# Kernel tuning notes

Measured on AMD Instinct MI355X. Metric: run time of the kernel, lower is better.

Reference implementation:

```python
import jax, jax.numpy as jnp
import numpy as np
from jax import lax

SCALES = [2 ** i for i in range(9)]  # h_grid_global(9, 2**8): dyadic scales 1..256
EPS = 2e-5


def conv1d(x, w, dil, pad):
    # x: [B, Cin, X], w: [Cout, Cin, k]; 'same'-style padding pad on each side, rhs dilation dil
    return lax.conv_general_dilated(x, w, window_strides=(1,), padding=[(pad, pad)],
                                    rhs_dilation=(dil,), dimension_numbers=('NCH', 'OIH', 'NCH'))


def maxpool2_x(x):
    # max pool kernel=2 stride=2 over last (spatial) axis, floor mode like torch
    L = x.shape[-1]
    L2 = (L // 2) * 2
    x = x[..., :L2]
    return jnp.max(x.reshape(x.shape[:-1] + (L2 // 2, 2)), axis=-1)


def lift_conv(x, w):
    k = w.shape[-1]
    outs = [conv1d(x, w, s, s * (k // 2)) / s for s in SCALES]
    return jnp.stack(outs, axis=2)


def gg_conv(x, w):
    # GConvGG with h_crop: x [B, Cin, H, X], w [Cout, Cin, nh=3, k] -> [B, Cout, H-2, X]
    # output scale index i uses input scale slabs i..i+2, x-dilation = scale_i, 1/scale_i normalization
    B, Cin, H, X = x.shape
    Cout, _, nh, k = w.shape
    wf = w.reshape(Cout, Cin * nh, k)
    outs = []
    for i in range(H - nh + 1):
        xi = x[:, :, i:i + nh, :].reshape(B, Cin * nh, X)
        s = SCALES[i]
        outs.append(conv1d(xi, wf, s, s * (k // 2)) / s)
    return jnp.stack(outs, axis=2)


def batchnorm(x, g, b):
    # BatchNorm2d (training batch stats, biased var) over [B, C, H, X]
    m = jnp.mean(x, axis=(0, 2, 3), keepdims=True)
    v = jnp.mean((x - m) ** 2, axis=(0, 2, 3), keepdims=True)
    gb = g[None, :, None, None]
    bb = b[None, :, None, None]
    return gb * (x - m) * lax.rsqrt(v + EPS) + bb


def _winit(key, shape):
    fan = int(np.prod(shape[1:]))
    return jax.random.normal(key, shape, dtype=jnp.float32) * (fan ** -0.5)


def setup_inputs() -> dict:
    key = jax.random.key(0)
    ks = jax.random.split(key, 12)
    B = 4096
    nc = 12
    x = jax.random.normal(ks[0], (B, 100, 6), dtype=jnp.float32)
    inp = {
        'x': x,
        'w1': _winit(ks[1], (nc, 6, 7)),
        'w2': _winit(ks[2], (nc * 2, nc, 3, 5)),
        'w3': _winit(ks[3], (nc * 4, nc * 2, 3, 5)),
        'w4': _winit(ks[4], (nc * 8, nc * 4, 3, 3)),
        'g1': jnp.ones((nc,), jnp.float32), 'b1': jnp.zeros((nc,), jnp.float32),
        'g2': jnp.ones((nc * 2,), jnp.float32), 'b2': jnp.zeros((nc * 2,), jnp.float32),
        'g3': jnp.ones((nc * 4,), jnp.float32), 'b3': jnp.zeros((nc * 4,), jnp.float32),
        'g4': jnp.ones((nc * 8,), jnp.float32), 'b4': jnp.zeros((nc * 8,), jnp.float32),
        'f1w': _winit(ks[5], (nc * 8, nc * 8 * 3)), 'f1b': jnp.zeros((nc * 8,), jnp.float32),
        'f2w': _winit(ks[6], (nc * 4, nc * 8)), 'f2b': jnp.zeros((nc * 4,), jnp.float32),
        'f3w': _winit(ks[7], (6, nc * 4)), 'f3b': jnp.zeros((6,), jnp.float32),
    }
    return inp


def reference(x, w1, w2, w3, w4, g1, b1, g2, b2, g3, b3, g4, b4,
              f1w, f1b, f2w, f2b, f3w, f3b):
    h = jnp.transpose(x, (0, 2, 1))          # [B, 6, 100]
    h = lift_conv(h, w1)                     # [B, 12, 9, 100]
    h = maxpool2_x(h)                        # [B, 12, 9, 50]
    h = batchnorm(jax.nn.relu(h), g1, b1)
    h = maxpool2_x(h)                        # [B, 12, 9, 25]
    h = gg_conv(h, w2)                       # [B, 24, 7, 25]
    h = maxpool2_x(h)                        # [B, 24, 7, 12]
    h = batchnorm(jax.nn.relu(h), g2, b2)
    h = maxpool2_x(h)                        # [B, 24, 7, 6]
    h = gg_conv(h, w3)                       # [B, 48, 5, 6]
    h = maxpool2_x(h)                        # [B, 48, 5, 3]
    h = batchnorm(jax.nn.relu(h), g3, b3)
    h = gg_conv(h, w4)                       # [B, 96, 3, 3]
    h = maxpool2_x(h)                        # [B, 96, 3, 1]
    h = batchnorm(jax.nn.relu(h), g4, b4)
    h = h.reshape(h.shape[0], -1)            # [B, 288]
    h = h @ f1w.T + f1b                      # dropout is identity in eval
    h = h @ f2w.T + f2b
    return h @ f3w.T + f3b                   # [B, 6]
```

## Files before the change

kernel.cpp:

```cpp
#include <hip/hip_runtime.h>
#include <hip/hip_fp16.h>

#define EPSBN 2e-5f

typedef _Float16 hf2 __attribute__((ext_vector_type(2)));
typedef _Float16 hf4 __attribute__((ext_vector_type(4)));
typedef _Float16 hf8 __attribute__((ext_vector_type(8)));
union U8 { hf8 v; hf2 p[4]; };

static __device__ __forceinline__ float fdot2h(hf2 a, hf2 b, float c) {
  return __builtin_amdgcn_fdot2(a, b, c, false);
}
static __device__ __forceinline__ unsigned pk(float a, float b) {
  union { __half2 h; unsigned u; } u;
  u.h = __floats2half2_rn(a, b);
  return u.u;
}
static __device__ __forceinline__ float2 uph(unsigned v) {
  union { unsigned u; __half2 h; } x; x.u = v;
  return __half22float2(x.h);
}

#define NB1 4
template<int SI>
__device__ __forceinline__ void s1_si(const unsigned* __restrict__ xsu, int bb, int t0,
    const unsigned* __restrict__ wlu, int o0, bool act, int b,
    __half* __restrict__ r1, float& ts0, float& tq0, float& ts1, float& tq1) {
  constexpr int S = 1 << SI;
  float a0[10], a1[10];
#pragma unroll
  for (int k = 0; k < 10; ++k) { a0[k] = 0.f; a1[k] = 0.f; }
#pragma unroll 1
  for (int cp = 0; cp < 3; ++cp) {
    const hf2* xr = (const hf2*)xsu + (bb * 3 + cp) * 296 + 96 + t0;
    const unsigned* wp = wlu + cp * 84;
#pragma unroll
    for (int j = 0; j < 7; ++j) {
      const int off = S * (j - 3);
      if (off < -96 || off > 98) continue;
      const int offE = off & ~1;
      const int sh = off & 1;
      hf2 w0 = *(const hf2*)(wp + j * 12 + o0);
      hf2 w1 = *(const hf2*)(wp + j * 12 + o0 + 1);
      hf2 xv[12];
#pragma unroll
      for (int q = 0; q < 6; ++q) {
        hf4 bufq = *(const hf4*)(xr + offE + 2 * q);
        xv[2 * q] = bufq.lo; xv[2 * q + 1] = bufq.hi;
      }
#pragma unroll
      for (int k = 0; k < 10; ++k) {
        a0[k] = fdot2h(xv[sh + k], w0, a0[k]);
        a1[k] = fdot2h(xv[sh + k], w1, a1[k]);
      }
    }
  }
  if (act) {
    const float inv = 1.0f / (float)S;
    size_t rb = ((size_t)b * 12 + o0) * 9 + SI;
#pragma unroll
    for (int u = 0; u < 5; ++u) {
      float v0 = fmaxf(fmaxf(a0[2 * u], a0[2 * u + 1]) * inv, 0.f);
      float v1 = fmaxf(fmaxf(a1[2 * u], a1[2 * u + 1]) * inv, 0.f);
      r1[rb * 50 + (t0 >> 1) + u] = __float2half_rn(v0);
      r1[(rb + 9) * 50 + (t0 >> 1) + u] = __float2half_rn(v1);
      ts0 += v0; tq0 += v0 * v0; ts1 += v1; tq1 += v1 * v1;
    }
  }
}

__global__ __launch_bounds__(256) void k_lift(const float* __restrict__ x,
    const float* __restrict__ w1, const float* __restrict__ w2,
    const float* __restrict__ w3, const float* __restrict__ w4,
    __half* __restrict__ W2P, __half* __restrict__ W3P, __half* __restrict__ W4P,
    __half* __restrict__ r1, float* __restrict__ sum, float* __restrict__ sq) {
  __shared__ __align__(16) unsigned xsu[NB1 * 888];
  __shared__ __align__(16) unsigned wlu[252];
  __shared__ float ssum[12], ssq[12];
  int b0 = blockIdx.x * NB1, tid = threadIdx.x;
  {
    int gi = blockIdx.x * 256 + tid;
    if (gi < 4320) {
      int ci = gi & 1, r = gi >> 1, o = r % 24, j = (r / 24) % 5, h = (r / 120) % 3, cp = r / 360;
      int c = 2 * cp + ci;
      W2P[gi] = __float2half_rn(w2[((o * 12 + c) * 3 + h) * 5 + j]);
    } else if (gi < 21600) {
      int k = gi - 4320;
      int ci = k & 1, r = k >> 1, o = r % 48, j = (r / 48) % 5, h = (r / 240) % 3, cp = r / 720;
      int c = 2 * cp + ci;
      W3P[k] = __float2half_rn(w3[((o * 24 + c) * 3 + h) * 5 + j]);
    } else if (gi < 63072) {
      int k = gi - 21600;
      int ci = k & 1, r = k >> 1, o48 = r % 48, j = (r / 48) % 3, h = (r / 144) % 3;
      int cp = (r / 432) % 24, ch = r / 10368, c = 2 * cp + ci, o = ch * 48 + o48;
      W4P[k] = __float2half_rn(w4[((o * 48 + c) * 3 + h) * 3 + j]);
    }
  }
  for (int i = tid; i < NB1 * 888; i += 256) xsu[i] = 0u;
  for (int i = tid; i < 252; i += 256) {
    int cp = i / 84, j = (i % 84) / 12, o = i % 12;
    wlu[i] = pk(w1[(o * 6 + 2 * cp) * 7 + j], w1[(o * 6 + 2 * cp + 1) * 7 + j]);
  }
  if (tid < 12) { ssum[tid] = 0.f; ssq[tid] = 0.f; }
  __syncthreads();
  __half* xsh = (__half*)xsu;
  for (int i = tid; i < NB1 * 600; i += 256) {
    int bb = i / 600, f = i % 600, t = f / 6, c = f % 6;
    xsh[((bb * 3 + (c >> 1)) * 296 + 96 + t) * 2 + (c & 1)] =
        __float2half_rn(x[(size_t)(b0 + bb) * 600 + f]);
  }
  __syncthreads();
  bool act = tid < 240;
  int task = act ? tid : 0;
  int bb = task / 60, r = task % 60;
  int op = r / 10, tc = r % 10;
  int o0 = op * 2, t0 = tc * 10;
  int b = b0 + bb;
  float ts0 = 0.f, tq0 = 0.f, ts1 = 0.f, tq1 = 0.f;
  s1_si<0>(xsu, bb, t0, wlu, o0, act, b, r1, ts0, tq0, ts1, tq1);
  s1_si<1>(xsu, bb, t0, wlu, o0, act, b, r1, ts0, tq0, ts1, tq1);
  s1_si<2>(xsu, bb, t0, wlu, o0, act, b, r1, ts0, tq0, ts1, tq1);
  s1_si<3>(xsu, bb, t0, wlu, o0, act, b, r1, ts0, tq0, ts1, tq1);
  s1_si<4>(xsu, bb, t0, wlu, o0, act, b, r1, ts0, tq0, ts1, tq1);
  s1_si<5>(xsu, bb, t0, wlu, o0, act, b, r1, ts0, tq0, ts1, tq1);
  s1_si<6>(xsu, bb, t0, wlu, o0, act, b, r1, ts0, tq0, ts1, tq1);
  s1_si<7>(xsu, bb, t0, wlu, o0, act, b, r1, ts0, tq0, ts1, tq1);
  s1_si<8>(xsu, bb, t0, wlu, o0, act, b, r1, ts0, tq0, ts1, tq1);
  if (act) {
    atomicAdd(&ssum[o0], ts0); atomicAdd(&ssq[o0], tq0);
    atomicAdd(&ssum[o0 + 1], ts1); atomicAdd(&ssq[o0 + 1], tq1);
  }
  __syncthreads();
  if (tid < 12) { atomicAdd(&sum[tid], ssum[tid]); atomicAdd(&sq[tid], ssq[tid]); }
}

#define NB2 5
template<int S, int I2>
__device__ __forceinline__ void s2_do(const unsigned* __restrict__ abu,
    const unsigned* __restrict__ wlu, int op, bool act, int b,
    unsigned* __restrict__ r2p, float& ts0, float& tq0, float& ts1, float& tq1) {
  float acc0[24], acc1[24];
#pragma unroll
  for (int t = 0; t < 24; ++t) { acc0[t] = 0.f; acc1[t] = 0.f; }
#pragma unroll 1
  for (int cp = 0; cp < 6; ++cp) {
#pragma unroll
    for (int h = 0; h < 3; ++h) {
      const unsigned* ar = abu + (cp * 9 + I2 + h) * 28;
      hf2 rr[28];
#pragma unroll
      for (int q = 0; q < 7; ++q) {
        U8 u; u.v = *(const hf8*)(ar + 4 * q);
        rr[4 * q] = u.p[0]; rr[4 * q + 1] = u.p[1];
        rr[4 * q + 2] = u.p[2]; rr[4 * q + 3] = u.p[3];
      }
      const unsigned* wp = wlu + ((cp * 3 + h) * 5) * 24 + op * 2;
#pragma unroll
      for (int j = 0; j < 5; ++j) {
        const int off = S * (j - 2);
        if (off <= -25 || off >= 25) continue;
        hf4 w01 = *(const hf4*)(wp + j * 24);
        hf2 w0 = w01.lo, w1 = w01.hi;
#pragma unroll
        for (int t = 0; t < 24; ++t) {
          if (t + off >= 0 && t + off < 25) {
            acc0[t] = fdot2h(rr[t + off], w0, acc0[t]);
            acc1[t] = fdot2h(rr[t + off], w1, acc1[t]);
          }
        }
      }
    }
  }
  if (act) {
    const float inv = 1.0f / (float)S;
    unsigned* pd = r2p + ((size_t)b * 12 + op) * 42 + I2 * 6;
    float m0 = 0.f, m1 = 0.f;
#pragma unroll
    for (int u = 0; u < 12; ++u) {
      float v0 = fmaxf(fmaxf(acc0[2 * u], acc0[2 * u + 1]) * inv, 0.f);
      float v1 = fmaxf(fmaxf(acc1[2 * u], acc1[2 * u + 1]) * inv, 0.f);
      ts0 += v0; tq0 += v0 * v0; ts1 += v1; tq1 += v1 * v1;
      if ((u & 1) == 0) { m0 = v0; m1 = v1; }
      else pd[u >> 1] = pk(fmaxf(m0, v0), fmaxf(m1, v1));
    }
  }
}

__global__ __launch_bounds__(256) void k_stage2(const __half* __restrict__ r1,
    const __half* __restrict__ W2P,
    const float* __restrict__ SUM, const float* __restrict__ SQ,
    const float* __restrict__ g, const float* __restrict__ bbn, float invN,
    unsigned* __restrict__ r2p, float* __restrict__ sum, float* __restrict__ sq, int B) {
  __shared__ __align__(16) unsigned asu[NB2 * 1512];
  __shared__ __align__(16) unsigned wlu[2160];
  __shared__ float ssum[24], ssq[24];
  __shared__ float scf[12], shf[12];
  int b0 = blockIdx.x * NB2, tid = threadIdx.x;
  if (tid < 12) {
    float m = SUM[tid] * invN;
    float v = SQ[tid] * invN - m * m;
    float scale = g[tid] * rsqrtf(v + EPSBN);
    scf[tid] = scale; shf[tid] = bbn[tid] - m * scale;
    ssum[tid] = 0.f; ssq[tid] = 0.f;
    ssum[tid + 12] = 0.f; ssq[tid + 12] = 0.f;
  }
  __syncthreads();
  for (int i = tid; i < NB2 * 1350; i += 256) {
    int bb = i / 1350, s = i % 1350;
    if (b0 + bb < B) {
      int cp = s / 225, rem = s % 225, row = rem / 25, t = rem % 25;
      int c0 = 2 * cp, c1 = c0 + 1;
      float2 a0 = __half22float2(*(const __half2*)(r1 +
          (((size_t)(b0 + bb) * 12 + c0) * 9 + row) * 50 + 2 * t));
      float2 a1 = __half22float2(*(const __half2*)(r1 +
          (((size_t)(b0 + bb) * 12 + c1) * 9 + row) * 50 + 2 * t));
      float v0 = fmaxf(a0.x, a0.y) * scf[c0] + shf[c0];
      float v1 = fmaxf(a1.x, a1.y) * scf[c1] + shf[c1];
      asu[bb * 1512 + (cp * 9 + row) * 28 + t] = pk(v0, v1);
    }
  }
  for (int i = tid; i < 540; i += 256)
    ((uint4*)wlu)[i] = ((const uint4*)W2P)[i];
  __syncthreads();
  int wv = tid >> 6, lane = tid & 63;
  int bb = lane / 12, op = lane % 12;
  bool act = (lane < 60) && (b0 + bb < B);
  if (bb > 4) bb = 4;
  const unsigned* abu = asu + bb * 1512;
  int b = b0 + bb;
  float ts0 = 0.f, tq0 = 0.f, ts1 = 0.f, tq1 = 0.f;
  if (wv == 0) {
    s2_do<1, 0>(abu, wlu, op, act, b, r2p, ts0, tq0, ts1, tq1);
  } else if (wv == 1) {
    s2_do<2, 1>(abu, wlu, op, act, b, r2p, ts0, tq0, ts1, tq1);
    s2_do<64, 6>(abu, wlu, op, act, b, r2p, ts0, tq0, ts1, tq1);
  } else if (wv == 2) {
    s2_do<4, 2>(abu, wlu, op, act, b, r2p, ts0, tq0, ts1, tq1);
    s2_do<32, 5>(abu, wlu, op, act, b, r2p, ts0, tq0, ts1, tq1);
  } else {
    s2_do<8, 3>(abu, wlu, op, act, b, r2p, ts0, tq0, ts1, tq1);
    s2_do<16, 4>(abu, wlu, op, act, b, r2p, ts0, tq0, ts1, tq1);
  }
  if (act) {
    int o0 = op * 2;
    atomicAdd(&ssum[o0], ts0); atomicAdd(&ssq[o0], tq0);
    atomicAdd(&ssum[o0 + 1], ts1); atomicAdd(&ssq[o0 + 1], tq1);
  }
  __syncthreads();
  if (tid < 24) { atomicAdd(&sum[tid], ssum[tid]); atomicAdd(&sq[tid], ssq[tid]); }
}

#define NB3 8
template<int I2>
__device__ __forceinline__ void s3h(const hf2* __restrict__ rr, int h,
    const hf2* __restrict__ w0, const hf2* __restrict__ w1, float* __restrict__ acc) {
  constexpr int S = 1 << I2;
  const int base = (I2 + h) * 6;
#pragma unroll
  for (int j = 0; j < 5; ++j) {
    const int off = S * (j - 2);
    if (off <= -6 || off >= 6) continue;
#pragma unroll
    for (int t = 0; t < 6; ++t) {
      if (t + off >= 0 && t + off < 6) {
        acc[t] = fdot2h(rr[base + t + off], w0[j], acc[t]);
        acc[6 + t] = fdot2h(rr[base + t + off], w1[j], acc[6 + t]);
      }
    }
  }
}

__global__ __launch_bounds__(256) void k_stage3(const unsigned* __restrict__ r2p,
    const __half* __restrict__ W3P,
    const float* __restrict__ SUM, const float* __restrict__ SQ,
    const float* __restrict__ g, const float* __restrict__ bbn, float invN,
    unsigned* __restrict__ r3, float* __restrict__ sum, float* __restrict__ sq) {
  __shared__ __align__(16) unsigned asu[NB3 * 536];
  __shared__ __align__(16) unsigned wlu[8640];
  __shared__ float ssum[48], ssq[48];
  __shared__ float scf[24], shf[24];
  int b0 = blockIdx.x * NB3, tid = threadIdx.x;
  if (tid < 24) {
    float m = SUM[tid] * invN;
    float v = SQ[tid] * invN - m * m;
    float scale = g[tid] * rsqrtf(v + EPSBN);
    scf[tid] = scale; shf[tid] = bbn[tid] - m * scale;
  }
  if (tid < 48) { ssum[tid] = 0.f; ssq[tid] = 0.f; }
  __syncthreads();
  for (int i = tid; i < NB3 * 504; i += 256) {
    int bb = i / 504, f = i % 504, cp = f / 42, r42 = f % 42;
    int c0 = 2 * cp, c1 = c0 + 1;
    float2 a = uph(r2p[(size_t)(b0 + bb) * 504 + f]);
    asu[bb * 536 + cp * 44 + r42] = pk(a.x * scf[c0] + shf[c0], a.y * scf[c1] + shf[c1]);
  }
  for (int i = tid; i < 2160; i += 256)
    ((uint4*)wlu)[i] = ((const uint4*)W3P)[i];
  __syncthreads();
  bool act = tid < 192;
  int bb = act ? tid / 24 : 0, op = tid % 24;
  int b = b0 + bb;
  if (act) {
    float acc[60];
#pragma unroll
    for (int k = 0; k < 60; ++k) acc[k] = 0.f;
#pragma unroll 1
    for (int cp = 0; cp < 12; ++cp) {
      const unsigned* ar = asu + bb * 536 + cp * 44;
      hf2 rr[44];
#pragma unroll
      for (int q = 0; q < 11; ++q) {
        U8 u; u.v = *(const hf8*)(ar + 4 * q);
        rr[4 * q] = u.p[0]; rr[4 * q + 1] = u.p[1];
        rr[4 * q + 2] = u.p[2]; rr[4 * q + 3] = u.p[3];
      }
#pragma unroll
      for (int h = 0; h < 3; ++h) {
        const unsigned* wp = wlu + (cp * 15 + h * 5) * 48 + op * 2;
        hf2 w0[5], w1[5];
#pragma unroll
        for (int j = 0; j < 5; ++j) {
          hf4 w01 = *(const hf4*)(wp + j * 48);
          w0[j] = w01.lo; w1[j] = w01.hi;
        }
        s3h<0>(rr, h, w0, w1, acc);
        s3h<1>(rr, h, w0, w1, acc + 12);
        s3h<2>(rr, h, w0, w1, acc + 24);
        s3h<3>(rr, h, w0, w1, acc + 36);
        s3h<4>(rr, h, w0, w1, acc + 48);
      }
    }
    float ts0 = 0.f, tq0 = 0.f, ts1 = 0.f, tq1 = 0.f;
    int ob = op * 2;
#pragma unroll
    for (int i2 = 0; i2 < 5; ++i2) {
      const float inv = 1.0f / (float)(1 << i2);
      size_t rb = ((size_t)b * 24 + op) * 15 + i2 * 3;
#pragma unroll
      for (int u = 0; u < 3; ++u) {
        float v0 = fmaxf(fmaxf(acc[i2 * 12 + 2 * u], acc[i2 * 12 + 2 * u + 1]) * inv, 0.f);
        float v1 = fmaxf(fmaxf(acc[i2 * 12 + 6 + 2 * u], acc[i2 * 12 + 7 + 2 * u]) * inv, 0.f);
        r3[rb + u] = pk(v0, v1);
        ts0 += v0; tq0 += v0 * v0; ts1 += v1; tq1 += v1 * v1;
      }
    }
    atomicAdd(&ssum[ob], ts0); atomicAdd(&ssq[ob], tq0);
    atomicAdd(&ssum[ob + 1], ts1); atomicAdd(&ssq[ob + 1], tq1);
  }
  __syncthreads();
  if (tid < 48) { atomicAdd(&sum[tid], ssum[tid]); atomicAdd(&sq[tid], ssq[tid]); }
}

#define NB4 8
template<int I2>
__device__ __forceinline__ void s4h(const hf2* __restrict__ rr, int h,
    const hf2* __restrict__ w0, const hf2* __restrict__ w1, float* __restrict__ acc) {
  constexpr int S = 1 << I2;
  const int base = (I2 + h) * 3;
#pragma unroll
  for (int j = 0; j < 3; ++j) {
    const int off = S * (j - 1);
    if (off <= -3 || off >= 3) continue;
    if (off >= 0) {
      acc[0] = fdot2h(rr[base + off], w0[j], acc[0]);
      acc[2] = fdot2h(rr[base + off], w1[j], acc[2]);
    }
    const int i1 = 1 + off;
    if (i1 >= 0 && i1 < 3) {
      acc[1] = fdot2h(rr[base + i1], w0[j], acc[1]);
      acc[3] = fdot2h(rr[base + i1], w1[j], acc[3]);
    }
  }
}

__global__ __launch_bounds__(256) void k_stage4(const unsigned* __restrict__ r3,
    const __half* __restrict__ W4P,
    const float* __restrict__ SUM, const float* __restrict__ SQ,
    const float* __restrict__ g, const float* __restrict__ bbn, float invN,
    float* __restrict__ r4, float* __restrict__ sum, float* __restrict__ sq) {
  __shared__ __align__(16) unsigned asu[NB4 * 392];
  __shared__ __align__(16) unsigned wlu[10368];
  __shared__ float ssum[96], ssq[96];
  __shared__ float scf[48], shf[48];
  int b0 = blockIdx.x * NB4, tid = threadIdx.x;
  if (tid < 48) {
    float m = SUM[tid] * invN;
    float v = SQ[tid] * invN - m * m;
    float scale = g[tid] * rsqrtf(v + EPSBN);
    scf[tid] = scale; shf[tid] = bbn[tid] - m * scale;
  }
  if (tid < 96) { ssum[tid] = 0.f; ssq[tid] = 0.f; }
  __syncthreads();
  for (int i = tid; i < NB4 * 360; i += 256) {
    int bb = i / 360, f = i % 360, cp = f / 15, r15 = f % 15;
    int c0 = 2 * cp, c1 = c0 + 1;
    float2 a = uph(r3[(size_t)(b0 + bb) * 360 + f]);
    asu[bb * 392 + cp * 16 + r15] = pk(a.x * scf[c0] + shf[c0], a.y * scf[c1] + shf[c1]);
  }
  bool act = tid < 192;
  int bb = act ? tid / 24 : 0, op = tid % 24;
  int b = b0 + bb;
  for (int chunk = 0; chunk < 2; ++chunk) {
    __syncthreads();
    for (int i = tid; i < 2592; i += 256)
      ((uint4*)wlu)[i] = ((const uint4*)W4P)[chunk * 2592 + i];
    __syncthreads();
    if (act) {
      float acc[12];
#pragma unroll
      for (int k = 0; k < 12; ++k) acc[k] = 0.f;
#pragma unroll 1
      for (int cp = 0; cp < 24; ++cp) {
        const unsigned* ar = asu + bb * 392 + cp * 16;
        hf2 rr[16];
#pragma unroll
        for (int q = 0; q < 4; ++q) {
          U8 u; u.v = *(const hf8*)(ar + 4 * q);
          rr[4 * q] = u.p[0]; rr[4 * q + 1] = u.p[1];
          rr[4 * q + 2] = u.p[2]; rr[4 * q + 3] = u.p[3];
        }
#pragma unroll
        for (int h = 0; h < 3; ++h) {
          const unsigned* wp = wlu + ((cp * 3 + h) * 3) * 48 + op * 2;
          hf2 w0[3], w1[3];
#pragma unroll
          for (int j = 0; j < 3; ++j) {
            hf4 w01 = *(const hf4*)(wp + j * 48);
            w0[j] = w01.lo; w1[j] = w01.hi;
          }
          s4h<0>(rr, h, w0, w1, acc);
          s4h<1>(rr, h, w0, w1, acc + 4);
          s4h<2>(rr, h, w0, w1, acc + 8);
        }
      }
      int o0 = chunk * 48 + op * 2;
#pragma unroll
      for (int oo = 0; oo < 2; ++oo) {
        float ts = 0.f, tq = 0.f;
#pragma unroll
        for (int i2 = 0; i2 < 3; ++i2) {
          const float inv = 1.0f / (float)(1 << i2);
          float v = fmaxf(fmaxf(acc[i2 * 4 + oo * 2], acc[i2 * 4 + oo * 2 + 1]) * inv, 0.f);
          r4[(size_t)b * 288 + (o0 + oo) * 3 + i2] = v;
          ts += v; tq += v * v;
        }
        atomicAdd(&ssum[o0 + oo], ts); atomicAdd(&ssq[o0 + oo], tq);
      }
    }
  }
  __syncthreads();
  if (tid < 96) { atomicAdd(&sum[tid], ssum[tid]); atomicAdd(&sq[tid], ssq[tid]); }
}

__global__ __launch_bounds__(256) void k_fc(const float* __restrict__ r4,
    const float* __restrict__ SUM, const float* __restrict__ SQ,
    const float* __restrict__ g, const float* __restrict__ bbn, float invN,
    const float* __restrict__ f1w, const float* __restrict__ f1b,
    const float* __restrict__ f2w, const float* __restrict__ f2b,
    const float* __restrict__ f3w, const float* __restrict__ f3b,
    float* __restrict__ out) {
  __shared__ float v[4][288];
  __shared__ float h1[4][96];
  __shared__ float h2[4][48];
  __shared__ float scf[96], shf[96];
  int b0 = blockIdx.x * 4, tid = threadIdx.x;
  if (tid < 96) {
    float m = SUM[tid] * invN;
    float vv = SQ[tid] * invN - m * m;
    float scale = g[tid] * rsqrtf(vv + EPSBN);
    scf[tid] = scale; shf[tid] = bbn[tid] - m * scale;
  }
  __syncthreads();
  for (int i = tid; i < 4 * 288; i += 256) {
    int bb = i / 288, f = i % 288, c = f / 3;
    v[bb][f] = r4[(size_t)(b0 + bb) * 288 + f] * scf[c] + shf[c];
  }
  __syncthreads();
  for (int d = tid; d < 384; d += 256) {
    int o = d >> 2, bb = d & 3;
    const float* wr = &f1w[o * 288];
    const float* vv = v[bb];
    float acc = f1b[o];
    for (int f = 0; f < 288; ++f) acc += wr[f] * vv[f];
    h1[bb][o] = acc;
  }
  __syncthreads();
  if (tid < 192) {
    int o = tid >> 2, bb = tid & 3;
    const float* wr = &f2w[o * 96];
    float acc = f2b[o];
    for (int f = 0; f < 96; ++f) acc += wr[f] * h1[bb][f];
    h2[bb][o] = acc;
  }
  __syncthreads();
  if (tid < 24) {
    int o = tid >> 2, bb = tid & 3;
    const float* wr = &f3w[o * 48];
    float acc = f3b[o];
    for (int f = 0; f < 48; ++f) acc += wr[f] * h2[bb][f];
    out[(size_t)(b0 + bb) * 6 + o] = acc;
  }
}

extern "C" void kernel_launch(void* const* d_in, const int* in_sizes, int n_in,
                              void* d_out, int out_size, void* d_ws, size_t ws_size,
                              hipStream_t stream) {
  const float* x   = (const float*)d_in[0];
  const float* w1  = (const float*)d_in[1];
  const float* w2  = (const float*)d_in[2];
  const float* w3  = (const float*)d_in[3];
  const float* w4  = (const float*)d_in[4];
  const float* g1  = (const float*)d_in[5];
  const float* b1  = (const float*)d_in[6];
  const float* g2  = (const float*)d_in[7];
  const float* b2  = (const float*)d_in[8];
  const float* g3  = (const float*)d_in[9];
  const float* b3  = (const float*)d_in[10];
  const float* g4  = (const float*)d_in[11];
  const float* b4  = (const float*)d_in[12];
  const float* f1w = (const float*)d_in[13];
  const float* f1b = (const float*)d_in[14];
  const float* f2w = (const float*)d_in[15];
  const float* f2b = (const float*)d_in[16];
  const float* f3w = (const float*)d_in[17];
  const float* f3b = (const float*)d_in[18];
  float* out = (float*)d_out;
  float* ws = (float*)d_ws;

  const int B = 4096;
  float* SUM1 = ws + 0;   float* SQ1 = ws + 12;
  float* SUM2 = ws + 24;  float* SQ2 = ws + 48;
  float* SUM3 = ws + 72;  float* SQ3 = ws + 120;
  float* SUM4 = ws + 168; float* SQ4 = ws + 264;
  __half* H0  = (__half*)(ws + 1024);
  __half* W2P = H0;
  __half* W3P = H0 + 4320;
  __half* W4P = H0 + 21600;
  __half* R1h = H0 + 65536;
  unsigned* R2P = (unsigned*)(R1h + (size_t)B * 5400);
  unsigned* R3D = (unsigned*)R1h;
  float*  R4  = (float*)(R2P + (size_t)B * 504);

  hipMemsetAsync(d_ws, 0, 384 * sizeof(float), stream);

  k_lift<<<B / NB1, 256, 0, stream>>>(x, w1, w2, w3, w4, W2P, W3P, W4P, R1h, SUM1, SQ1);
  k_stage2<<<(B + NB2 - 1) / NB2, 256, 0, stream>>>(R1h, W2P, SUM1, SQ1, g1, b1,
      1.0f / (float)(B * 450), R2P, SUM2, SQ2, B);
  k_stage3<<<B / NB3, 256, 0, stream>>>(R2P, W3P, SUM2, SQ2, g2, b2,
      1.0f / (float)(B * 84), R3D, SUM3, SQ3);
  k_stage4<<<B / NB4, 256, 0, stream>>>(R3D, W4P, SUM3, SQ3, g3, b3,
      1.0f / (float)(B * 15), R4, SUM4, SQ4);
  k_fc<<<B / 4, 256, 0, stream>>>(R4, SUM4, SQ4, g4, b4,
      1.0f / (float)(B * 3), f1w, f1b, f2w, f2b, f3w, f3b, out);
}
```

Measured before the change: 300.4 us.

## Rewrite stage-2 group conv with MFMA 16x16x32 f16 and repacked weights

Replaces the fdot2-based stage-2 scale-group convolution with an MFMA formulation. Weights are prepacked into a fragment-ready layout with output channels padded to 32 and the (h,j,c) reduction padded to 256. Activations are gathered per lane with shift offsets and zero-masked. The block grows to 512 threads and 8 batch items, with 42 work units spread across the waves. Padding and masking waste part of the matrix throughput, and the scattered per-lane LDS gathers add overhead in exchange for the tensor-unit use.

```diff
diff --git a/kernel.cpp b/kernel.cpp
--- a/kernel.cpp
+++ b/kernel.cpp
@@ -6,7 +6,9 @@
 typedef _Float16 hf2 __attribute__((ext_vector_type(2)));
 typedef _Float16 hf4 __attribute__((ext_vector_type(4)));
 typedef _Float16 hf8 __attribute__((ext_vector_type(8)));
+typedef float f32x4 __attribute__((ext_vector_type(4)));
 union U8 { hf8 v; hf2 p[4]; };
+union BFR { unsigned u[4]; hf8 v; };
 
 static __device__ __forceinline__ float fdot2h(hf2 a, hf2 b, float c) {
   return __builtin_amdgcn_fdot2(a, b, c, false);
@@ -72,7 +74,7 @@
 __global__ __launch_bounds__(256) void k_lift(const float* __restrict__ x,
     const float* __restrict__ w1, const float* __restrict__ w2,
     const float* __restrict__ w3, const float* __restrict__ w4,
-    __half* __restrict__ W2P, __half* __restrict__ W3P, __half* __restrict__ W4P,
+    __half* __restrict__ W2M, __half* __restrict__ W3P, __half* __restrict__ W4P,
     __half* __restrict__ r1, float* __restrict__ sum, float* __restrict__ sq) {
   __shared__ __align__(16) unsigned xsu[NB1 * 888];
   __shared__ __align__(16) unsigned wlu[252];
@@ -80,17 +82,22 @@
   int b0 = blockIdx.x * NB1, tid = threadIdx.x;
   {
     int gi = blockIdx.x * 256 + tid;
-    if (gi < 4320) {
-      int ci = gi & 1, r = gi >> 1, o = r % 24, j = (r / 24) % 5, h = (r / 120) % 3, cp = r / 360;
-      int c = 2 * cp + ci;
-      W2P[gi] = __float2half_rn(w2[((o * 12 + c) * 3 + h) * 5 + j]);
-    } else if (gi < 21600) {
-      int k = gi - 4320;
+    if (gi < 8192) {
+      int i = gi & 7, L = (gi >> 3) & 63, s = (gi >> 9) & 7, mt = gi >> 12;
+      int o = mt * 16 + (L & 15);
+      int sub = ((L >> 4) << 3) + i;
+      int hj = 2 * s + (sub >> 4), c = sub & 15;
+      float v = 0.f;
+      if (o < 24 && c < 12 && hj < 15)
+        v = w2[((o * 12 + c) * 3 + (hj / 5)) * 5 + (hj % 5)];
+      W2M[gi] = __float2half_rn(v);
+    } else if (gi < 25472) {
+      int k = gi - 8192;
       int ci = k & 1, r = k >> 1, o = r % 48, j = (r / 48) % 5, h = (r / 240) % 3, cp = r / 720;
       int c = 2 * cp + ci;
       W3P[k] = __float2half_rn(w3[((o * 24 + c) * 3 + h) * 5 + j]);
-    } else if (gi < 63072) {
-      int k = gi - 21600;
+    } else if (gi < 66944) {
+      int k = gi - 25472;
       int ci = k & 1, r = k >> 1, o48 = r % 48, j = (r / 48) % 3, h = (r / 144) % 3;
       int cp = (r / 432) % 24, ch = r / 10368, c = 2 * cp + ci, o = ch * 48 + o48;
       W4P[k] = __float2half_rn(w4[((o * 48 + c) * 3 + h) * 3 + j]);
@@ -134,117 +141,122 @@
   if (tid < 12) { atomicAdd(&sum[tid], ssum[tid]); atomicAdd(&sq[tid], ssq[tid]); }
 }
 
-#define NB2 5
-template<int S, int I2>
-__device__ __forceinline__ void s2_do(const unsigned* __restrict__ abu,
-    const unsigned* __restrict__ wlu, int op, bool act, int b,
-    unsigned* __restrict__ r2p, float& ts0, float& tq0, float& ts1, float& tq1) {
-  float acc0[24], acc1[24];
-#pragma unroll
-  for (int t = 0; t < 24; ++t) { acc0[t] = 0.f; acc1[t] = 0.f; }
-#pragma unroll 1
-  for (int cp = 0; cp < 6; ++cp) {
-#pragma unroll
-    for (int h = 0; h < 3; ++h) {
-      const unsigned* ar = abu + (cp * 9 + I2 + h) * 28;
-      hf2 rr[28];
-#pragma unroll
-      for (int q = 0; q < 7; ++q) {
-        U8 u; u.v = *(const hf8*)(ar + 4 * q);
-        rr[4 * q] = u.p[0]; rr[4 * q + 1] = u.p[1];
-        rr[4 * q + 2] = u.p[2]; rr[4 * q + 3] = u.p[3];
-      }
-      const unsigned* wp = wlu + ((cp * 3 + h) * 5) * 24 + op * 2;
-#pragma unroll
-      for (int j = 0; j < 5; ++j) {
-        const int off = S * (j - 2);
-        if (off <= -25 || off >= 25) continue;
-        hf4 w01 = *(const hf4*)(wp + j * 24);
-        hf2 w0 = w01.lo, w1 = w01.hi;
-#pragma unroll
-        for (int t = 0; t < 24; ++t) {
-          if (t + off >= 0 && t + off < 25) {
-            acc0[t] = fdot2h(rr[t + off], w0, acc0[t]);
-            acc1[t] = fdot2h(rr[t + off], w1, acc1[t]);
-          }
-        }
-      }
-    }
-  }
-  if (act) {
-    const float inv = 1.0f / (float)S;
-    unsigned* pd = r2p + ((size_t)b * 12 + op) * 42 + I2 * 6;
-    float m0 = 0.f, m1 = 0.f;
-#pragma unroll
-    for (int u = 0; u < 12; ++u) {
-      float v0 = fmaxf(fmaxf(acc0[2 * u], acc0[2 * u + 1]) * inv, 0.f);
-      float v1 = fmaxf(fmaxf(acc1[2 * u], acc1[2 * u + 1]) * inv, 0.f);
-      ts0 += v0; tq0 += v0 * v0; ts1 += v1; tq1 += v1 * v1;
-      if ((u & 1) == 0) { m0 = v0; m1 = v1; }
-      else pd[u >> 1] = pk(fmaxf(m0, v0), fmaxf(m1, v1));
-    }
-  }
-}
-
-__global__ __launch_bounds__(256) void k_stage2(const __half* __restrict__ r1,
-    const __half* __restrict__ W2P,
+
+__global__ __launch_bounds__(512) void k_stage2(const __half* __restrict__ r1,
+    const __half* __restrict__ W2M,
     const float* __restrict__ SUM, const float* __restrict__ SQ,
     const float* __restrict__ g, const float* __restrict__ bbn, float invN,
-    unsigned* __restrict__ r2p, float* __restrict__ sum, float* __restrict__ sq, int B) {
-  __shared__ __align__(16) unsigned asu[NB2 * 1512];
-  __shared__ __align__(16) unsigned wlu[2160];
+    unsigned* __restrict__ r2p, float* __restrict__ sum, float* __restrict__ sq) {
+  __shared__ __align__(16) unsigned asu[8 * 1512 + 768];
+  __shared__ __align__(16) unsigned wm[4096];
   __shared__ float ssum[24], ssq[24];
   __shared__ float scf[12], shf[12];
-  int b0 = blockIdx.x * NB2, tid = threadIdx.x;
+  int b0 = blockIdx.x * 8, tid = threadIdx.x;
   if (tid < 12) {
     float m = SUM[tid] * invN;
     float v = SQ[tid] * invN - m * m;
     float scale = g[tid] * rsqrtf(v + EPSBN);
     scf[tid] = scale; shf[tid] = bbn[tid] - m * scale;
-    ssum[tid] = 0.f; ssq[tid] = 0.f;
-    ssum[tid + 12] = 0.f; ssq[tid + 12] = 0.f;
-  }
-  __syncthreads();
-  for (int i = tid; i < NB2 * 1350; i += 256) {
+  }
+  if (tid < 24) { ssum[tid] = 0.f; ssq[tid] = 0.f; }
+  __syncthreads();
+  for (int i = tid; i < 8 * 1350; i += 512) {
     int bb = i / 1350, s = i % 1350;
-    if (b0 + bb < B) {
-      int cp = s / 225, rem = s % 225, row = rem / 25, t = rem % 25;
-      int c0 = 2 * cp, c1 = c0 + 1;
-      float2 a0 = __half22float2(*(const __half2*)(r1 +
-          (((size_t)(b0 + bb) * 12 + c0) * 9 + row) * 50 + 2 * t));
-      float2 a1 = __half22float2(*(const __half2*)(r1 +
-          (((size_t)(b0 + bb) * 12 + c1) * 9 + row) * 50 + 2 * t));
-      float v0 = fmaxf(a0.x, a0.y) * scf[c0] + shf[c0];
-      float v1 = fmaxf(a1.x, a1.y) * scf[c1] + shf[c1];
-      asu[bb * 1512 + (cp * 9 + row) * 28 + t] = pk(v0, v1);
-    }
-  }
-  for (int i = tid; i < 540; i += 256)
-    ((uint4*)wlu)[i] = ((const uint4*)W2P)[i];
-  __syncthreads();
-  int wv = tid >> 6, lane = tid & 63;
-  int bb = lane / 12, op = lane % 12;
-  bool act = (lane < 60) && (b0 + bb < B);
-  if (bb > 4) bb = 4;
-  const unsigned* abu = asu + bb * 1512;
+    int cp = s / 225, rem = s % 225, row = rem / 25, t = rem % 25;
+    int c0 = 2 * cp, c1 = c0 + 1;
+    float2 a0 = __half22float2(*(const __half2*)(r1 +
+        (((size_t)(b0 + bb) * 12 + c0) * 9 + row) * 50 + 2 * t));
+    float2 a1 = __half22float2(*(const __half2*)(r1 +
+        (((size_t)(b0 + bb) * 12 + c1) * 9 + row) * 50 + 2 * t));
+    float v0 = fmaxf(a0.x, a0.y) * scf[c0] + shf[c0];
+    float v1 = fmaxf(a1.x, a1.y) * scf[c1] + shf[c1];
+    asu[bb * 1512 + (cp * 9 + row) * 28 + t] = pk(v0, v1);
+  }
+  for (int i = tid; i < 1024; i += 512)
+    ((uint4*)wm)[i] = ((const uint4*)W2M)[i];
+  __syncthreads();
+  int wave = tid >> 6, lane = tid & 63;
+  int n = lane & 15, q = lane >> 4;
+  int bb = n >> 1, tp = n & 1;
+  int qh = q >> 1;
+  int ql = q & 1;
   int b = b0 + bb;
-  float ts0 = 0.f, tq0 = 0.f, ts1 = 0.f, tq1 = 0.f;
-  if (wv == 0) {
-    s2_do<1, 0>(abu, wlu, op, act, b, r2p, ts0, tq0, ts1, tq1);
-  } else if (wv == 1) {
-    s2_do<2, 1>(abu, wlu, op, act, b, r2p, ts0, tq0, ts1, tq1);
-    s2_do<64, 6>(abu, wlu, op, act, b, r2p, ts0, tq0, ts1, tq1);
-  } else if (wv == 2) {
-    s2_do<4, 2>(abu, wlu, op, act, b, r2p, ts0, tq0, ts1, tq1);
-    s2_do<32, 5>(abu, wlu, op, act, b, r2p, ts0, tq0, ts1, tq1);
-  } else {
-    s2_do<8, 3>(abu, wlu, op, act, b, r2p, ts0, tq0, ts1, tq1);
-    s2_do<16, 4>(abu, wlu, op, act, b, r2p, ts0, tq0, ts1, tq1);
-  }
-  if (act) {
-    int o0 = op * 2;
-    atomicAdd(&ssum[o0], ts0); atomicAdd(&ssq[o0], tq0);
-    atomicAdd(&ssum[o0 + 1], ts1); atomicAdd(&ssq[o0 + 1], tq1);
+  float s8[8], q8[8];
+#pragma unroll
+  for (int k = 0; k < 8; ++k) { s8[k] = 0.f; q8[k] = 0.f; }
+  int abase = bb * 1512 + ql * 1008;
+  for (int unit = wave; unit < 42; unit += 8) {
+    int i2 = unit / 6, up = unit % 6;
+    float inv = 1.0f / (float)(1 << i2);
+    f32x4 acc[2][2];
+#pragma unroll
+    for (int a = 0; a < 2; ++a)
+#pragma unroll
+      for (int m = 0; m < 2; ++m) acc[a][m] = (f32x4){0.f, 0.f, 0.f, 0.f};
+#pragma unroll 1
+    for (int uu = 0; uu < 2; ++uu) {
+      int tbase = 2 * (2 * up + uu) + tp;
+#pragma unroll 1
+      for (int s = 0; s < 8; ++s) {
+        int hj0 = 2 * s, hj1 = 2 * s + 1;
+        int off0 = ((hj0 % 5) - 2) << i2;
+        int off1 = ((hj1 % 5) - 2) << i2;
+        bool live0 = (off0 > -24) && (off0 < 25);
+        bool live1 = (hj1 < 15) && (off1 > -24) && (off1 < 25);
+        if (!live0 && !live1) continue;
+        int off = qh ? off1 : off0;
+        int row = i2 + (qh ? (hj1 / 5) : (hj0 / 5));
+        int tcur = tbase + off;
+        bool val = (tcur >= 0) && (tcur < 25) && (qh ? live1 : live0);
+        int tcl = min(max(tcur, 0), 24);
+        int ad = abase + row * 28 + tcl;
+        unsigned d0 = asu[ad], d1 = asu[ad + 252];
+        unsigned d2 = asu[ad + 504], d3 = asu[ad + 756];
+        bool v23 = val && (ql == 0);
+        BFR bf;
+        bf.u[0] = val ? d0 : 0u;
+        bf.u[1] = val ? d1 : 0u;
+        bf.u[2] = v23 ? d2 : 0u;
+        bf.u[3] = v23 ? d3 : 0u;
+#pragma unroll
+        for (int mt = 0; mt < 2; ++mt) {
+          hf8 wf = *(const hf8*)&wm[(mt * 8 + s) * 256 + lane * 4];
+          acc[uu][mt] = __builtin_amdgcn_mfma_f32_16x16x32_f16(wf, bf.v, acc[uu][mt], 0, 0, 0);
+        }
+      }
+    }
+#pragma unroll
+    for (int mt = 0; mt < 2; ++mt) {
+      float po[4];
+#pragma unroll
+      for (int reg = 0; reg < 4; ++reg) {
+        float a0 = acc[0][mt][reg];
+        float v0 = fmaxf(fmaxf(a0, __shfl_xor(a0, 1)) * inv, 0.f);
+        float a1 = acc[1][mt][reg];
+        float v1 = fmaxf(fmaxf(a1, __shfl_xor(a1, 1)) * inv, 0.f);
+        s8[mt * 4 + reg] += v0 + v1;
+        q8[mt * 4 + reg] += v0 * v0 + v1 * v1;
+        po[reg] = fmaxf(v0, v1);
+      }
+      if (tp == 0 && (mt == 0 || q < 2)) {
+        int opb = mt * 8 + q * 2;
+        size_t ab2 = ((size_t)b * 12 + opb) * 42 + i2 * 6 + up;
+        r2p[ab2] = pk(po[0], po[1]);
+        r2p[ab2 + 42] = pk(po[2], po[3]);
+      }
+    }
+  }
+  if (tp == 0) {
+#pragma unroll
+    for (int mt = 0; mt < 2; ++mt)
+#pragma unroll
+      for (int reg = 0; reg < 4; ++reg) {
+        int o = mt * 16 + q * 4 + reg;
+        if (o < 24) {
+          atomicAdd(&ssum[o], s8[mt * 4 + reg]);
+          atomicAdd(&ssq[o], q8[mt * 4 + reg]);
+        }
+      }
   }
   __syncthreads();
   if (tid < 24) { atomicAdd(&sum[tid], ssum[tid]); atomicAdd(&sq[tid], ssq[tid]); }
@@ -533,19 +545,19 @@
   float* SUM3 = ws + 72;  float* SQ3 = ws + 120;
   float* SUM4 = ws + 168; float* SQ4 = ws + 264;
   __half* H0  = (__half*)(ws + 1024);
-  __half* W2P = H0;
-  __half* W3P = H0 + 4320;
-  __half* W4P = H0 + 21600;
-  __half* R1h = H0 + 65536;
+  __half* W2M = H0;
+  __half* W3P = H0 + 8192;
+  __half* W4P = H0 + 25472;
+  __half* R1h = H0 + 81920;
   unsigned* R2P = (unsigned*)(R1h + (size_t)B * 5400);
   unsigned* R3D = (unsigned*)R1h;
   float*  R4  = (float*)(R2P + (size_t)B * 504);
 
   hipMemsetAsync(d_ws, 0, 384 * sizeof(float), stream);
 
-  k_lift<<<B / NB1, 256, 0, stream>>>(x, w1, w2, w3, w4, W2P, W3P, W4P, R1h, SUM1, SQ1);
-  k_stage2<<<(B + NB2 - 1) / NB2, 256, 0, stream>>>(R1h, W2P, SUM1, SQ1, g1, b1,
-      1.0f / (float)(B * 450), R2P, SUM2, SQ2, B);
+  k_lift<<<B / NB1, 256, 0, stream>>>(x, w1, w2, w3, w4, W2M, W3P, W4P, R1h, SUM1, SQ1);
+  k_stage2<<<B / 8, 512, 0, stream>>>(R1h, W2M, SUM1, SQ1, g1, b1,
+      1.0f / (float)(B * 450), R2P, SUM2, SQ2);
   k_stage3<<<B / NB3, 256, 0, stream>>>(R2P, W3P, SUM2, SQ2, g2, b2,
       1.0f / (float)(B * 84), R3D, SUM3, SQ3);
   k_stage4<<<B / NB4, 256, 0, stream>>>(R3D, W4P, SUM3, SQ3, g3, b3,
```

Result: slower. 401.7 us (+33.7%).

## Remap stage3/stage4 threads to one output channel each with fewer samples per block

Applied to the files above, without the earlier changes.

Stages 3 and 4 now give each thread a single output channel instead of a pair, and halve the samples per block from 8 to 4, so each block still uses 192 active threads. This halves per-thread accumulators, which cuts register pressure and may raise occupancy, and doubles the block count to give more parallelism. In exchange, each activation row is loaded from LDS by twice as many threads, and stage 3 needs a lane shuffle to pack channel pairs before storing. All threads, including the idle ones, now run the compute loop, and only the stores and atomics are guarded.

```diff
diff --git a/kernel.cpp b/kernel.cpp
--- a/kernel.cpp
+++ b/kernel.cpp
@@ -250,10 +250,10 @@
   if (tid < 24) { atomicAdd(&sum[tid], ssum[tid]); atomicAdd(&sq[tid], ssq[tid]); }
 }
 
-#define NB3 8
+#define NB3 4
 template<int I2>
-__device__ __forceinline__ void s3h(const hf2* __restrict__ rr, int h,
-    const hf2* __restrict__ w0, const hf2* __restrict__ w1, float* __restrict__ acc) {
+__device__ __forceinline__ void s3s(const hf2* __restrict__ rr, int h,
+    const hf2* __restrict__ w, float* __restrict__ acc) {
   constexpr int S = 1 << I2;
   const int base = (I2 + h) * 6;
 #pragma unroll
@@ -262,10 +262,8 @@
     if (off <= -6 || off >= 6) continue;
 #pragma unroll
     for (int t = 0; t < 6; ++t) {
-      if (t + off >= 0 && t + off < 6) {
-        acc[t] = fdot2h(rr[base + t + off], w0[j], acc[t]);
-        acc[6 + t] = fdot2h(rr[base + t + off], w1[j], acc[6 + t]);
-      }
+      if (t + off >= 0 && t + off < 6)
+        acc[t] = fdot2h(rr[base + t + off], w[j], acc[t]);
     }
   }
 }
@@ -298,78 +296,65 @@
     ((uint4*)wlu)[i] = ((const uint4*)W3P)[i];
   __syncthreads();
   bool act = tid < 192;
-  int bb = act ? tid / 24 : 0, op = tid % 24;
+  int bb = act ? tid / 48 : 3, ox = tid % 48;
   int b = b0 + bb;
-  if (act) {
-    float acc[60];
-#pragma unroll
-    for (int k = 0; k < 60; ++k) acc[k] = 0.f;
+  float acc[30];
+#pragma unroll
+  for (int k = 0; k < 30; ++k) acc[k] = 0.f;
 #pragma unroll 1
-    for (int cp = 0; cp < 12; ++cp) {
-      const unsigned* ar = asu + bb * 536 + cp * 44;
-      hf2 rr[44];
-#pragma unroll
-      for (int q = 0; q < 11; ++q) {
-        U8 u; u.v = *(const hf8*)(ar + 4 * q);
-        rr[4 * q] = u.p[0]; rr[4 * q + 1] = u.p[1];
-        rr[4 * q + 2] = u.p[2]; rr[4 * q + 3] = u.p[3];
-      }
-#pragma unroll
-      for (int h = 0; h < 3; ++h) {
-        const unsigned* wp = wlu + (cp * 15 + h * 5) * 48 + op * 2;
-        hf2 w0[5], w1[5];
-#pragma unroll
-        for (int j = 0; j < 5; ++j) {
-          hf4 w01 = *(const hf4*)(wp + j * 48);
-          w0[j] = w01.lo; w1[j] = w01.hi;
-        }
-        s3h<0>(rr, h, w0, w1, acc);
-        s3h<1>(rr, h, w0, w1, acc + 12);
-        s3h<2>(rr, h, w0, w1, acc + 24);
-        s3h<3>(rr, h, w0, w1, acc + 36);
-        s3h<4>(rr, h, w0, w1, acc + 48);
-      }
-    }
-    float ts0 = 0.f, tq0 = 0.f, ts1 = 0.f, tq1 = 0.f;
-    int ob = op * 2;
-#pragma unroll
-    for (int i2 = 0; i2 < 5; ++i2) {
-      const float inv = 1.0f / (float)(1 << i2);
-      size_t rb = ((size_t)b * 24 + op) * 15 + i2 * 3;
-#pragma unroll
-      for (int u = 0; u < 3; ++u) {
-        float v0 = fmaxf(fmaxf(acc[i2 * 12 + 2 * u], acc[i2 * 12 + 2 * u + 1]) * inv, 0.f);
-        float v1 = fmaxf(fmaxf(acc[i2 * 12 + 6 + 2 * u], acc[i2 * 12 + 7 + 2 * u]) * inv, 0.f);
-        r3[rb + u] = pk(v0, v1);
-        ts0 += v0; tq0 += v0 * v0; ts1 += v1; tq1 += v1 * v1;
-      }
-    }
-    atomicAdd(&ssum[ob], ts0); atomicAdd(&ssq[ob], tq0);
-    atomicAdd(&ssum[ob + 1], ts1); atomicAdd(&ssq[ob + 1], tq1);
-  }
+  for (int cp = 0; cp < 12; ++cp) {
+    const unsigned* ar = asu + bb * 536 + cp * 44;
+    hf2 rr[44];
+#pragma unroll
+    for (int q = 0; q < 11; ++q) {
+      U8 u; u.v = *(const hf8*)(ar + 4 * q);
+      rr[4 * q] = u.p[0]; rr[4 * q + 1] = u.p[1];
+      rr[4 * q + 2] = u.p[2]; rr[4 * q + 3] = u.p[3];
+    }
+#pragma unroll
+    for (int h = 0; h < 3; ++h) {
+      hf2 w[5];
+#pragma unroll
+      for (int j = 0; j < 5; ++j)
+        w[j] = *(const hf2*)(wlu + (cp * 15 + h * 5 + j) * 48 + ox);
+      s3s<0>(rr, h, w, acc);
+      s3s<1>(rr, h, w, acc + 6);
+      s3s<2>(rr, h, w, acc + 12);
+      s3s<3>(rr, h, w, acc + 18);
+      s3s<4>(rr, h, w, acc + 24);
+    }
+  }
+  float ts = 0.f, tq = 0.f;
+#pragma unroll
+  for (int i2 = 0; i2 < 5; ++i2) {
+    const float inv = 1.0f / (float)(1 << i2);
+    size_t rb = ((size_t)b * 24 + (ox >> 1)) * 15 + i2 * 3;
+#pragma unroll
+    for (int u = 0; u < 3; ++u) {
+      float v = fmaxf(fmaxf(acc[i2 * 6 + 2 * u], acc[i2 * 6 + 2 * u + 1]) * inv, 0.f);
+      float vo = __shfl_xor(v, 1);
+      ts += v; tq += v * v;
+      if (act && (ox & 1) == 0) r3[rb + u] = pk(v, vo);
+    }
+  }
+  if (act) { atomicAdd(&ssum[ox], ts); atomicAdd(&ssq[ox], tq); }
   __syncthreads();
   if (tid < 48) { atomicAdd(&sum[tid], ssum[tid]); atomicAdd(&sq[tid], ssq[tid]); }
 }
 
-#define NB4 8
+#define NB4 4
 template<int I2>
-__device__ __forceinline__ void s4h(const hf2* __restrict__ rr, int h,
-    const hf2* __restrict__ w0, const hf2* __restrict__ w1, float* __restrict__ acc) {
+__device__ __forceinline__ void s4s(const hf2* __restrict__ rr, int h,
+    const hf2* __restrict__ w, float* __restrict__ acc) {
   constexpr int S = 1 << I2;
   const int base = (I2 + h) * 3;
 #pragma unroll
   for (int j = 0; j < 3; ++j) {
     const int off = S * (j - 1);
     if (off <= -3 || off >= 3) continue;
-    if (off >= 0) {
-      acc[0] = fdot2h(rr[base + off], w0[j], acc[0]);
-      acc[2] = fdot2h(rr[base + off], w1[j], acc[2]);
-    }
+    if (off >= 0) acc[0] = fdot2h(rr[base + off], w[j], acc[0]);
     const int i1 = 1 + off;
-    if (i1 >= 0 && i1 < 3) {
-      acc[1] = fdot2h(rr[base + i1], w0[j], acc[1]);
-      acc[3] = fdot2h(rr[base + i1], w1[j], acc[3]);
-    }
+    if (i1 >= 0 && i1 < 3) acc[1] = fdot2h(rr[base + i1], w[j], acc[1]);
   }
 }
 
@@ -398,54 +383,48 @@
     asu[bb * 392 + cp * 16 + r15] = pk(a.x * scf[c0] + shf[c0], a.y * scf[c1] + shf[c1]);
   }
   bool act = tid < 192;
-  int bb = act ? tid / 24 : 0, op = tid % 24;
+  int bb = act ? tid / 48 : 3, ox = tid % 48;
   int b = b0 + bb;
   for (int chunk = 0; chunk < 2; ++chunk) {
     __syncthreads();
     for (int i = tid; i < 2592; i += 256)
       ((uint4*)wlu)[i] = ((const uint4*)W4P)[chunk * 2592 + i];
     __syncthreads();
+    float acc[6];
+#pragma unroll
+    for (int k = 0; k < 6; ++k) acc[k] = 0.f;
+#pragma unroll 1
+    for (int cp = 0; cp < 24; ++cp) {
+      const unsigned* ar = asu + bb * 392 + cp * 16;
+      hf2 rr[16];
+#pragma unroll
+      for (int q = 0; q < 4; ++q) {
+        U8 u; u.v = *(const hf8*)(ar + 4 * q);
+        rr[4 * q] = u.p[0]; rr[4 * q + 1] = u.p[1];
+        rr[4 * q + 2] = u.p[2]; rr[4 * q + 3] = u.p[3];
+      }
+#pragma unroll
+      for (int h = 0; h < 3; ++h) {
+        hf2 w[3];
+#pragma unroll
+        for (int j = 0; j < 3; ++j)
+          w[j] = *(const hf2*)(wlu + ((cp * 3 + h) * 3 + j) * 48 + ox);
+        s4s<0>(rr, h, w, acc);
+        s4s<1>(rr, h, w, acc + 2);
+        s4s<2>(rr, h, w, acc + 4);
+      }
+    }
     if (act) {
-      float acc[12];
-#pragma unroll
-      for (int k = 0; k < 12; ++k) acc[k] = 0.f;
-#pragma unroll 1
-      for (int cp = 0; cp < 24; ++cp) {
-        const unsigned* ar = asu + bb * 392 + cp * 16;
-        hf2 rr[16];
-#pragma unroll
-        for (int q = 0; q < 4; ++q) {
-          U8 u; u.v = *(const hf8*)(ar + 4 * q);
-          rr[4 * q] = u.p[0]; rr[4 * q + 1] = u.p[1];
-          rr[4 * q + 2] = u.p[2]; rr[4 * q + 3] = u.p[3];
-        }
-#pragma unroll
-        for (int h = 0; h < 3; ++h) {
-          const unsigned* wp = wlu + ((cp * 3 + h) * 3) * 48 + op * 2;
-          hf2 w0[3], w1[3];
-#pragma unroll
-          for (int j = 0; j < 3; ++j) {
-            hf4 w01 = *(const hf4*)(wp + j * 48);
-            w0[j] = w01.lo; w1[j] = w01.hi;
-          }
-          s4h<0>(rr, h, w0, w1, acc);
-          s4h<1>(rr, h, w0, w1, acc + 4);
-          s4h<2>(rr, h, w0, w1, acc + 8);
-        }
-      }
-      int o0 = chunk * 48 + op * 2;
-#pragma unroll
-      for (int oo = 0; oo < 2; ++oo) {
-        float ts = 0.f, tq = 0.f;
-#pragma unroll
-        for (int i2 = 0; i2 < 3; ++i2) {
-          const float inv = 1.0f / (float)(1 << i2);
-          float v = fmaxf(fmaxf(acc[i2 * 4 + oo * 2], acc[i2 * 4 + oo * 2 + 1]) * inv, 0.f);
-          r4[(size_t)b * 288 + (o0 + oo) * 3 + i2] = v;
-          ts += v; tq += v * v;
-        }
-        atomicAdd(&ssum[o0 + oo], ts); atomicAdd(&ssq[o0 + oo], tq);
-      }
+      int o = chunk * 48 + ox;
+      float ts = 0.f, tq = 0.f;
+#pragma unroll
+      for (int i2 = 0; i2 < 3; ++i2) {
+        const float inv = 1.0f / (float)(1 << i2);
+        float v = fmaxf(fmaxf(acc[i2 * 2], acc[i2 * 2 + 1]) * inv, 0.f);
+        r4[(size_t)b * 288 + o * 3 + i2] = v;
+        ts += v; tq += v * v;
+      }
+      atomicAdd(&ssum[o], ts); atomicAdd(&ssq[o], tq);
     }
   }
   __syncthreads();
```

After: 333.2 us. 10.9% more time.
